# Optimization experiments

Hardware: AMD Instinct MI355X
Metric: run time of the kernel (lower is better)

## Reference

```python
import jax, jax.numpy as jnp
import numpy as np

B, T, E, H = 4, 2048, 1024, 16
HD = E // H

def setup_inputs() -> dict:
    key = jax.random.key(0)
    ks = jax.random.split(key, 5)
    s = 1.0 / np.sqrt(E)
    return {
        "x": jax.random.normal(ks[0], (B, T, E), dtype=jnp.float32),
        "mask": jnp.zeros((B, T), dtype=bool),
        "qkv_w": jax.random.uniform(ks[1], (3 * E, E), jnp.float32, -s, s),
        "qkv_b": jax.random.uniform(ks[2], (3 * E,), jnp.float32, -s, s),
        "proj_w": jax.random.uniform(ks[3], (E, E), jnp.float32, -s, s),
        "proj_b": jax.random.uniform(ks[4], (E,), jnp.float32, -s, s),
    }

def reference(x, mask, qkv_w, qkv_b, proj_w, proj_b):
    b, t, e = x.shape
    qkv = x @ qkv_w.T + qkv_b                      # [b,t,3e]
    q, k, v = jnp.split(qkv, 3, axis=2)
    # [b,t,e] -> [b,h,t,hd]
    q = q.reshape(b, t, H, HD).transpose(0, 2, 1, 3)
    k = k.reshape(b, t, H, HD).transpose(0, 2, 1, 3)
    v = v.reshape(b, t, H, HD).transpose(0, 2, 1, 3)
    scale = 1.0 / np.sqrt(HD)
    attn = jnp.einsum('bhqd,bhkd->bhqk', q, k) * scale
    # mask: True -> -inf, broadcast over heads and query positions
    neg = jnp.where(mask, -jnp.inf, 0.0).astype(attn.dtype)  # [b,t]
    attn = attn + neg[:, None, None, :]
    attn = jax.nn.softmax(attn, axis=-1)
    # dropout layers in eval mode (deterministic reference)
    out = jnp.einsum('bhqk,bhkd->bhqd', attn, v)   # [b,h,t,hd]
    out = out.transpose(0, 2, 1, 3).reshape(b, t, e)
    return out @ proj_w.T + proj_b
```

## Files before the change

kernel.cpp:

```cpp
#include <hip/hip_runtime.h>
#include <stdint.h>

#define Bz  4
#define Tz  2048
#define Ez  1024
#define Hz  16
#define HDz 64
#define Mz  (Bz*Tz)

typedef short bf16x8 __attribute__((ext_vector_type(8)));
typedef float f32x4  __attribute__((ext_vector_type(4)));
typedef unsigned short u16;

__device__ __forceinline__ u16 f2bf(float f) {
  return (u16)((__builtin_bit_cast(uint32_t, f) + 0x8000u) >> 16);
}
__device__ __forceinline__ uint32_t pack2bf(float a, float b) {
  uint32_t ua = __builtin_bit_cast(uint32_t, a) + 0x8000u;
  uint32_t ub = __builtin_bit_cast(uint32_t, b) + 0x8000u;
  return __builtin_amdgcn_perm(ub, ua, 0x07060302u);
}

#if __has_builtin(__builtin_amdgcn_exp2f)
#define EXP2(x) __builtin_amdgcn_exp2f(x)
#else
#define EXP2(x) exp2f(x)
#endif

__device__ __forceinline__ void gl2lds16(const u16* g, u16* l) {
  __builtin_amdgcn_global_load_lds((const __attribute__((address_space(1))) void*)g,
                                   (__attribute__((address_space(3))) void*)l, 16, 0, 0);
}

__global__ void cvt_f32_bf16(const float* __restrict__ src, u16* __restrict__ dst, int n4) {
  int i = blockIdx.x * blockDim.x + threadIdx.x;
  if (i >= n4) return;
  float4 f = ((const float4*)src)[i];
  uint2 o;
  o.x = pack2bf(f.x, f.y);
  o.y = pack2bf(f.z, f.w);
  ((uint2*)dst)[i] = o;
}

template<int MODE>
__global__ __launch_bounds__(256, 2) void gemm_bt(
    const u16* __restrict__ A, const u16* __restrict__ Bw,
    const float* __restrict__ bias,
    u16* __restrict__ qo, u16* __restrict__ ko, u16* __restrict__ vto,
    float* __restrict__ fo)
{
  __shared__ u16 Ab[128*64];
  __shared__ u16 Bb[128*64];
  const int tid  = threadIdx.x;
  const int lane = tid & 63;
  const int wid  = tid >> 6;
  const int quad = lane >> 4;
  const int cl   = lane & 15;
  const int wm   = wid >> 1, wn = wid & 1;
  const int bm   = blockIdx.y * 128;
  const int bn   = blockIdx.x * 128;
  const int srow = lane >> 3;
  const int ssw  = lane & 7;

  f32x4 acc[4][4] = {};

  for (int kt = 0; kt < Ez; kt += 64) {
    __syncthreads();
#pragma unroll
    for (int s = 0; s < 4; ++s) {
      const int r  = wid*32 + s*8 + srow;
      const int cc = ssw ^ (r & 7);
      gl2lds16(A + (size_t)(bm + r)*Ez + kt + cc*8, &Ab[(wid*32 + s*8)*64]);
    }
#pragma unroll
    for (int s = 0; s < 4; ++s) {
      const int r  = wid*32 + s*8 + srow;
      const int cc = ssw ^ (r & 7);
      gl2lds16(Bw + (size_t)(bn + r)*Ez + kt + cc*8, &Bb[(wid*32 + s*8)*64]);
    }
    __syncthreads();
#pragma unroll
    for (int ks = 0; ks < 2; ++ks) {
      bf16x8 af[4], bfr[4];
#pragma unroll
      for (int mi = 0; mi < 4; ++mi) {
        const int row = wm*64 + mi*16 + cl;
        const int ch  = (ks*4 + quad) ^ (row & 7);
        af[mi] = *(const bf16x8*)&Ab[row*64 + ch*8];
      }
#pragma unroll
      for (int ni = 0; ni < 4; ++ni) {
        const int row = wn*64 + ni*16 + cl;
        const int ch  = (ks*4 + quad) ^ (row & 7);
        bfr[ni] = *(const bf16x8*)&Bb[row*64 + ch*8];
      }
#pragma unroll
      for (int mi = 0; mi < 4; ++mi)
#pragma unroll
        for (int ni = 0; ni < 4; ++ni)
          acc[mi][ni] = __builtin_amdgcn_mfma_f32_16x16x32_bf16(af[mi], bfr[ni], acc[mi][ni], 0, 0, 0);
    }
  }

  const float qsc = 0.125f * 1.4426950408889634f;
#pragma unroll
  for (int ni = 0; ni < 4; ++ni) {
    const int n   = bn + wn*64 + ni*16 + cl;
    const float bv = bias[n];
#pragma unroll
    for (int mi = 0; mi < 4; ++mi) {
      const int m0 = bm + wm*64 + mi*16 + quad*4;
      if (MODE == 0) {
        const int which = n >> 10;
        const int e = n & 1023;
        const int h = e >> 6, d = e & 63;
        const int b = m0 >> 11, t0 = m0 & 2047;
        if (which == 2) {
          uint2 pk;
          pk.x = pack2bf(acc[mi][ni][0] + bv, acc[mi][ni][1] + bv);
          pk.y = pack2bf(acc[mi][ni][2] + bv, acc[mi][ni][3] + bv);
          *(uint2*)&vto[(((size_t)(b*Hz + h))*HDz + d)*Tz + t0] = pk;
        } else {
#pragma unroll
          for (int r = 0; r < 4; ++r) {
            const int t = t0 + r;
            float val = acc[mi][ni][r] + bv;
            if (which == 0) qo[(((size_t)(b*Hz + h))*Tz + t)*HDz + d] = f2bf(val * qsc);
            else            ko[(((size_t)(b*Hz + h))*Tz + t)*HDz + d] = f2bf(val);
          }
        }
      } else {
#pragma unroll
        for (int r = 0; r < 4; ++r)
          fo[(size_t)(m0 + r)*Ez + n] = acc[mi][ni][r] + bv;
      }
    }
  }
}

__global__ __launch_bounds__(256, 4) void attn_flash(
    const u16* __restrict__ Q, const u16* __restrict__ K,
    const u16* __restrict__ Vt, const unsigned char* __restrict__ mask,
    u16* __restrict__ ctx)
{
  __shared__ u16 Kb[2][32*64];
  __shared__ u16 Vb[2][64*32];
  __shared__ u16 Pb[4*2*16*36];

  const int tid  = threadIdx.x;
  const int lane = tid & 63;
  const int wid  = tid >> 6;
  const int quad = lane >> 4;
  const int cl   = lane & 15;
  const int bh   = blockIdx.x;
  const int b    = bh >> 4;
  const int qrw  = blockIdx.y * 128 + wid * 32;
  u16* Pw = &Pb[wid * (2*16*36)];

  const int krow = wid*8  + (lane >> 3);
  const int kch  = (lane & 7) ^ (krow & 7);
  const int vrow = wid*16 + (lane >> 2);
  const int vch  = (lane & 3) ^ (vrow & 3);
  const u16* Kg = K  + ((size_t)bh*Tz + krow)*HDz + kch*8;
  const u16* Vg = Vt + ((size_t)bh*HDz + vrow)*Tz + vch*8;
  u16* KbL[2] = { &Kb[0][(wid*8)*64],  &Kb[1][(wid*8)*64]  };
  u16* VbL[2] = { &Vb[0][(wid*16)*32], &Vb[1][(wid*16)*32] };

  const unsigned char* mrow_p = mask + (size_t)b * Tz;
  bool domask;
  {
    const uint4* mp = (const uint4*)mrow_p;
    uint4 a = mp[lane*2], c = mp[lane*2 + 1];
    uint32_t any = a.x | a.y | a.z | a.w | c.x | c.y | c.z | c.w;
    domask = __any(any != 0);
  }

  bf16x8 aq[2][2];
#pragma unroll
  for (int qb = 0; qb < 2; ++qb) {
    const u16* Qg = Q + ((size_t)bh*Tz + qrw + qb*16 + cl)*HDz;
    aq[qb][0] = *(const bf16x8*)(Qg + quad*8);
    aq[qb][1] = *(const bf16x8*)(Qg + 32 + quad*8);
  }

  bf16x8 ones;
#pragma unroll
  for (int i = 0; i < 8; ++i) ones[i] = (short)0x3F80;

  f32x4 o[2][4] = {};
  f32x4 lacc[2] = {};

  gl2lds16(Kg, KbL[0]);
  gl2lds16(Vg, VbL[0]);

#pragma unroll 2
  for (int it = 0; it < 64; ++it) {
    const int bufc = it & 1;
    __syncthreads();
    if (it < 63) {
      gl2lds16(Kg + (size_t)(it+1)*32*HDz, KbL[bufc^1]);
      gl2lds16(Vg + (it+1)*32,             VbL[bufc^1]);
    }
    const u16* KB = &Kb[bufc][0];
    const u16* VB = &Vb[bufc][0];
    const int kt = it * 32;

    f32x4 st[2][2] = {};
#pragma unroll
    for (int kb = 0; kb < 2; ++kb) {
      bf16x8 kf[2];
#pragma unroll
      for (int nb = 0; nb < 2; ++nb) {
        const int row = nb*16 + cl;
        const int ch  = (kb*4 + quad) ^ (row & 7);
        kf[nb] = *(const bf16x8*)&KB[row*64 + ch*8];
      }
#pragma unroll
      for (int qb = 0; qb < 2; ++qb)
#pragma unroll
        for (int nb = 0; nb < 2; ++nb)
          st[qb][nb] = __builtin_amdgcn_mfma_f32_16x16x32_bf16(kf[nb], aq[qb][kb], st[qb][nb], 0, 0, 0);
    }

    if (domask) {
#pragma unroll
      for (int nb = 0; nb < 2; ++nb) {
        uint32_t mm = *(const uint32_t*)&mrow_p[kt + nb*16 + quad*4];
        if (mm) {
#pragma unroll
          for (int qb = 0; qb < 2; ++qb) {
            if (mm & 0x000000ffu) st[qb][nb][0] = -INFINITY;
            if (mm & 0x0000ff00u) st[qb][nb][1] = -INFINITY;
            if (mm & 0x00ff0000u) st[qb][nb][2] = -INFINITY;
            if (mm & 0xff000000u) st[qb][nb][3] = -INFINITY;
          }
        }
      }
    }

#pragma unroll
    for (int qb = 0; qb < 2; ++qb) {
      u16* Pq = Pw + qb * (16*36);
#pragma unroll
      for (int nb = 0; nb < 2; ++nb) {
        uint2 pk;
        pk.x = pack2bf(EXP2(st[qb][nb][0]), EXP2(st[qb][nb][1]));
        pk.y = pack2bf(EXP2(st[qb][nb][2]), EXP2(st[qb][nb][3]));
        *(uint2*)&Pq[cl*36 + (nb*4 + quad)*4] = pk;
      }
    }

    bf16x8 pf[2];
#pragma unroll
    for (int qb = 0; qb < 2; ++qb) {
      const u16* pr = &Pw[qb*(16*36) + cl*36 + quad*8];
      uint2 lo = *(const uint2*)pr;
      uint2 hi = *(const uint2*)(pr + 4);
      int4 pi = { (int)lo.x, (int)lo.y, (int)hi.x, (int)hi.y };
      pf[qb] = __builtin_bit_cast(bf16x8, pi);
      lacc[qb] = __builtin_amdgcn_mfma_f32_16x16x32_bf16(pf[qb], ones, lacc[qb], 0, 0, 0);
    }
#pragma unroll
    for (int db = 0; db < 4; ++db) {
      const int row = db*16 + cl;
      const int ch  = quad ^ (row & 3);
      bf16x8 bv = *(const bf16x8*)&VB[row*32 + ch*8];
#pragma unroll
      for (int qb = 0; qb < 2; ++qb)
        o[qb][db] = __builtin_amdgcn_mfma_f32_16x16x32_bf16(pf[qb], bv, o[qb][db], 0, 0, 0);
    }
  }

#pragma unroll
  for (int qb = 0; qb < 2; ++qb) {
#pragma unroll
    for (int r = 0; r < 4; ++r) {
      const float inv = 1.0f / lacc[qb][r];
      const int t = qrw + qb*16 + quad*4 + r;
      const size_t base = ((size_t)b*Tz + t)*Ez + (size_t)(bh & 15)*HDz;
#pragma unroll
      for (int db = 0; db < 4; ++db) {
        ctx[base + db*16 + cl] = f2bf(o[qb][db][r] * inv);
      }
    }
  }
}

extern "C" void kernel_launch(void* const* d_in, const int* in_sizes, int n_in,
                              void* d_out, int out_size, void* d_ws, size_t ws_size,
                              hipStream_t stream) {
  (void)in_sizes; (void)n_in; (void)out_size; (void)ws_size;
  const float* x      = (const float*)d_in[0];
  const unsigned char* mask = (const unsigned char*)d_in[1];
  const float* qkv_w  = (const float*)d_in[2];
  const float* qkv_b  = (const float*)d_in[3];
  const float* proj_w = (const float*)d_in[4];
  const float* proj_b = (const float*)d_in[5];
  float* out = (float*)d_out;

  char* ws = (char*)d_ws;
  u16* xb   = (u16*)(ws + 0);
  u16* wqb  = (u16*)(ws + 16777216);
  u16* wpb  = (u16*)(ws + 23068672);
  u16* Qb   = (u16*)(ws + 25165824);
  u16* Kb_  = (u16*)(ws + 41943040);
  u16* Vtb  = (u16*)(ws + 58720256);
  u16* ctxb = (u16*)(ws + 75497472);

  cvt_f32_bf16<<<8192, 256, 0, stream>>>(x,      xb,  2097152);
  cvt_f32_bf16<<<3072, 256, 0, stream>>>(qkv_w,  wqb,  786432);
  cvt_f32_bf16<<<1024, 256, 0, stream>>>(proj_w, wpb,  262144);

  gemm_bt<0><<<dim3(24, 64), 256, 0, stream>>>(xb, wqb, qkv_b, Qb, Kb_, Vtb, nullptr);
  attn_flash<<<dim3(64, 16), 256, 0, stream>>>(Qb, Kb_, Vtb, mask, ctxb);
  gemm_bt<1><<<dim3(8, 64), 256, 0, stream>>>(ctxb, wpb, proj_b, nullptr, nullptr, nullptr, out);
}
```

Baseline: 270.8 us.

## Double-buffer GEMM LDS tiles, merge conversion kernels, and reswizzle V tile

The GEMM kernel now keeps two LDS buffers, so the loads for the next K tile are issued before the MFMAs on the current one, which hides global-load latency behind compute and drops one barrier per iteration. The three fp32-to-bf16 conversion launches are merged into a single launch to cut launch overhead. The V tile swizzle in the attention kernel changes from row&3 to (row>>1)&3 to reduce LDS bank conflicts. LDS use in the GEMM doubles to 64KB per block, which may cut occupancy below the launch-bounds target of 2 blocks.

```diff
diff --git a/kernel.cpp b/kernel.cpp
--- a/kernel.cpp
+++ b/kernel.cpp
@@ -32,14 +32,22 @@
                                    (__attribute__((address_space(3))) void*)l, 16, 0, 0);
 }
 
-__global__ void cvt_f32_bf16(const float* __restrict__ src, u16* __restrict__ dst, int n4) {
-  int i = blockIdx.x * blockDim.x + threadIdx.x;
-  if (i >= n4) return;
-  float4 f = ((const float4*)src)[i];
+__global__ void cvt_f32_bf16_3(const float* __restrict__ s0, u16* __restrict__ d0, int n0,
+                               const float* __restrict__ s1, u16* __restrict__ d1, int n1,
+                               const float* __restrict__ s2, u16* __restrict__ d2, int n2) {
+  int j = blockIdx.x * blockDim.x + threadIdx.x;
+  const float* s; u16* d;
+  if (j < n0) { s = s0; d = d0; }
+  else {
+    j -= n0;
+    if (j < n1) { s = s1; d = d1; }
+    else { j -= n1; if (j >= n2) return; s = s2; d = d2; }
+  }
+  float4 f = ((const float4*)s)[j];
   uint2 o;
   o.x = pack2bf(f.x, f.y);
   o.y = pack2bf(f.z, f.w);
-  ((uint2*)dst)[i] = o;
+  ((uint2*)d)[j] = o;
 }
 
 template<int MODE>
@@ -49,8 +57,8 @@
     u16* __restrict__ qo, u16* __restrict__ ko, u16* __restrict__ vto,
     float* __restrict__ fo)
 {
-  __shared__ u16 Ab[128*64];
-  __shared__ u16 Bb[128*64];
+  __shared__ u16 Ab[2][128*64];
+  __shared__ u16 Bb[2][128*64];
   const int tid  = threadIdx.x;
   const int lane = tid & 63;
   const int wid  = tid >> 6;
@@ -64,21 +72,30 @@
 
   f32x4 acc[4][4] = {};
 
-  for (int kt = 0; kt < Ez; kt += 64) {
-    __syncthreads();
+  auto stage = [&](int kt, int buf) {
 #pragma unroll
     for (int s = 0; s < 4; ++s) {
       const int r  = wid*32 + s*8 + srow;
       const int cc = ssw ^ (r & 7);
-      gl2lds16(A + (size_t)(bm + r)*Ez + kt + cc*8, &Ab[(wid*32 + s*8)*64]);
+      gl2lds16(A + (size_t)(bm + r)*Ez + kt + cc*8, &Ab[buf][(wid*32 + s*8)*64]);
     }
 #pragma unroll
     for (int s = 0; s < 4; ++s) {
       const int r  = wid*32 + s*8 + srow;
       const int cc = ssw ^ (r & 7);
-      gl2lds16(Bw + (size_t)(bn + r)*Ez + kt + cc*8, &Bb[(wid*32 + s*8)*64]);
-    }
+      gl2lds16(Bw + (size_t)(bn + r)*Ez + kt + cc*8, &Bb[buf][(wid*32 + s*8)*64]);
+    }
+  };
+
+  stage(0, 0);
+
+#pragma unroll 2
+  for (int it = 0; it < 16; ++it) {
+    const int bufc = it & 1;
     __syncthreads();
+    if (it < 15) stage((it+1)*64, bufc^1);
+    const u16* AB = &Ab[bufc][0];
+    const u16* BB = &Bb[bufc][0];
 #pragma unroll
     for (int ks = 0; ks < 2; ++ks) {
       bf16x8 af[4], bfr[4];
@@ -86,13 +103,13 @@
       for (int mi = 0; mi < 4; ++mi) {
         const int row = wm*64 + mi*16 + cl;
         const int ch  = (ks*4 + quad) ^ (row & 7);
-        af[mi] = *(const bf16x8*)&Ab[row*64 + ch*8];
+        af[mi] = *(const bf16x8*)&AB[row*64 + ch*8];
       }
 #pragma unroll
       for (int ni = 0; ni < 4; ++ni) {
         const int row = wn*64 + ni*16 + cl;
         const int ch  = (ks*4 + quad) ^ (row & 7);
-        bfr[ni] = *(const bf16x8*)&Bb[row*64 + ch*8];
+        bfr[ni] = *(const bf16x8*)&BB[row*64 + ch*8];
       }
 #pragma unroll
       for (int mi = 0; mi < 4; ++mi)
@@ -160,7 +177,7 @@
   const int krow = wid*8  + (lane >> 3);
   const int kch  = (lane & 7) ^ (krow & 7);
   const int vrow = wid*16 + (lane >> 2);
-  const int vch  = (lane & 3) ^ (vrow & 3);
+  const int vch  = (lane & 3) ^ ((vrow >> 1) & 3);
   const u16* Kg = K  + ((size_t)bh*Tz + krow)*HDz + kch*8;
   const u16* Vg = Vt + ((size_t)bh*HDz + vrow)*Tz + vch*8;
   u16* KbL[2] = { &Kb[0][(wid*8)*64],  &Kb[1][(wid*8)*64]  };
@@ -263,7 +280,7 @@
 #pragma unroll
     for (int db = 0; db < 4; ++db) {
       const int row = db*16 + cl;
-      const int ch  = quad ^ (row & 3);
+      const int ch  = quad ^ ((row >> 1) & 3);
       bf16x8 bv = *(const bf16x8*)&VB[row*32 + ch*8];
 #pragma unroll
       for (int qb = 0; qb < 2; ++qb)
@@ -307,9 +324,9 @@
   u16* Vtb  = (u16*)(ws + 58720256);
   u16* ctxb = (u16*)(ws + 75497472);
 
-  cvt_f32_bf16<<<8192, 256, 0, stream>>>(x,      xb,  2097152);
-  cvt_f32_bf16<<<3072, 256, 0, stream>>>(qkv_w,  wqb,  786432);
-  cvt_f32_bf16<<<1024, 256, 0, stream>>>(proj_w, wpb,  262144);
+  cvt_f32_bf16_3<<<12288, 256, 0, stream>>>(x, xb, 2097152,
+                                            qkv_w, wqb, 786432,
+                                            proj_w, wpb, 262144);
 
   gemm_bt<0><<<dim3(24, 64), 256, 0, stream>>>(xb, wqb, qkv_b, Qb, Kb_, Vtb, nullptr);
   attn_flash<<<dim3(64, 16), 256, 0, stream>>>(Qb, Kb_, Vtb, mask, ctxb);
```

Result: faster. 265.4 us (-2.0%).
